# Performance work log

Hardware: AMD Instinct MI355X
Metric: run time of the kernel (lower is better)

## Reference

```python
import jax, jax.numpy as jnp
import numpy as np

B, N, C_CLASS, C_CHARGE, S_MAX = 128, 256, 5, 3, 300


def setup_inputs() -> dict:
    key = jax.random.key(0)
    ks = jax.random.split(key, 12)
    return {
        "particle_class": jax.random.randint(ks[0], (B, N), 0, C_CLASS),
        "particle_charge": jax.random.randint(ks[1], (B, N), 0, C_CHARGE),
        "n_particles": jax.random.randint(ks[2], (B,), 0, S_MAX),
        "pflow_class_logits": jax.random.normal(ks[3], (B, N, C_CLASS), jnp.float32),
        "pflow_charge_logits": jax.random.normal(ks[4], (B, N, C_CHARGE), jnp.float32),
        "particle_pos": jax.random.normal(ks[5], (B, N, 3), jnp.float32),
        "pflow_pos": jax.random.normal(ks[6], (B, N, 3), jnp.float32),
        "particle_mom": jax.random.normal(ks[7], (B, N, 3), jnp.float32),
        "pflow_mom": jax.random.normal(ks[8], (B, N, 3), jnp.float32),
        "particle_energy": jax.random.normal(ks[9], (B, N), jnp.float32),
        "pflow_energy": jax.random.normal(ks[10], (B, N), jnp.float32),
        "predicted_setsizes": jax.random.normal(ks[11], (B, N, S_MAX), jnp.float32),
    }


def _pairwise_nll(logits, labels):
    # logits: [B, Nq, C] (pflow/dst side), labels: [B, Np] int (particle/src side)
    # returns CE(dst_logits_j, src_label_i) for every pair -> [B, Np, Nq]
    logp = jax.nn.log_softmax(logits, axis=-1)            # [B, Nq, C]
    idx = labels[:, :, None, None]                        # [B, Np, 1, 1]
    return -jnp.take_along_axis(logp[:, None, :, :], idx, axis=3)[..., 0]


def reference(particle_class, particle_charge, n_particles,
              pflow_class_logits, pflow_charge_logits,
              particle_pos, pflow_pos, particle_mom, pflow_mom,
              particle_energy, pflow_energy, predicted_setsizes):
    # per-edge (full bipartite per event) pair losses -> [B, Np, Nq]
    class_l = _pairwise_nll(pflow_class_logits, particle_class)
    charge_l = _pairwise_nll(pflow_charge_logits, particle_charge)
    pos_l = jnp.linalg.norm(particle_pos[:, :, None, :] - pflow_pos[:, None, :, :], axis=-1)
    mom_l = jnp.linalg.norm(particle_mom[:, :, None, :] - pflow_mom[:, None, :, :], axis=-1)
    en_l = (particle_energy[:, :, None] - pflow_energy[:, None, :]) ** 2
    pair_loss = class_l + charge_l + pos_l + mom_l + en_l  # [B, Np, Nq]

    # segment-min over mailbox: per-pflow min over incoming particle edges,
    # per-particle min over incoming pflow edges
    min_per_pflow = pair_loss.min(axis=1)      # [B, Nq]
    min_per_particle = pair_loss.min(axis=2)   # [B, Np]

    particle_loss = min_per_particle.sum(axis=1).mean()
    pflow_loss = min_per_pflow.sum(axis=1).mean()

    # setsize: mean over pflow nodes per event, CE against true multiplicity
    setsize_logp = jax.nn.log_softmax(predicted_setsizes.mean(axis=1), axis=-1)  # [B, S]
    setsize_loss = -jnp.take_along_axis(setsize_logp, n_particles[:, None], axis=1)[:, 0].mean()

    loss = particle_loss + pflow_loss + setsize_loss
    return loss
```

## Files before the change

### kernel.cpp

```cpp
#include <hip/hip_runtime.h>
#include <math.h>

#define BQ 128
#define NQ 256
#define SMAX 300
#define CCLS 5
#define CCHG 3
#define TSTR 268
#define RSTR 12
#define INFV 3.0e38f

#define NBLK 256

#define W_COL 0
#define W_SC  65536
#define W_SS  65792

#define P_TAB   0
#define P_COLS  4020
#define P_ROWS  6068
#define P_RED   7604
#define P_PART  9652
#define SMEM_FLOATS 9656

__device__ __forceinline__ float fast_sqrtf(float x) {
    return __builtin_amdgcn_sqrtf(x);
}

__global__ __launch_bounds__(512, 2) void main_kernel(
    const int* __restrict__ p_class, const int* __restrict__ p_charge,
    const float* __restrict__ cls_logits, const float* __restrict__ chg_logits,
    const float* __restrict__ p_pos, const float* __restrict__ pf_pos,
    const float* __restrict__ p_mom, const float* __restrict__ pf_mom,
    const float* __restrict__ p_en, const float* __restrict__ pf_en,
    const float* __restrict__ setsizes, float* __restrict__ ws,
    float* __restrict__ out, int out_size)
{
    __shared__ float smem[SMEM_FLOATS];
    const int t   = threadIdx.x;
    const int blk = blockIdx.x;
    const int b   = blk >> 1;
    const int h   = blk & 1;
    const int base = b * NQ;

    float* s_tab  = smem + P_TAB;
    float* s_cols = smem + P_COLS;
    float* s_rows = smem + P_ROWS;
    float* s_red  = smem + P_RED;
    float* s_part = smem + P_PART;

    if (t < NQ) {
        const int gj = base + t;
        const float* cl = cls_logits + (size_t)gj * CCLS;
        float l0=cl[0], l1=cl[1], l2=cl[2], l3=cl[3], l4=cl[4];
        float mx = fmaxf(fmaxf(fmaxf(l0,l1),fmaxf(l2,l3)),l4);
        float lse = mx + __logf(__expf(l0-mx)+__expf(l1-mx)+__expf(l2-mx)+
                                __expf(l3-mx)+__expf(l4-mx));
        const float* gl = chg_logits + (size_t)gj * CCHG;
        float g0=gl[0], g1=gl[1], g2=gl[2];
        float gmx = fmaxf(fmaxf(g0,g1),g2);
        float glse = gmx + __logf(__expf(g0-gmx)+__expf(g1-gmx)+__expf(g2-gmx));
        float nc[CCLS] = {lse-l0, lse-l1, lse-l2, lse-l3, lse-l4};
        float ng[CCHG] = {glse-g0, glse-g1, glse-g2};
        #pragma unroll
        for (int c = 0; c < CCLS; ++c)
            #pragma unroll
            for (int g = 0; g < CCHG; ++g)
                s_tab[(c*CCHG+g)*TSTR + t] = nc[c] + ng[g];

        float* cr = &s_cols[t*8];
        cr[0]=pf_pos[gj*3+0]; cr[1]=pf_pos[gj*3+1]; cr[2]=pf_pos[gj*3+2];
        cr[3]=pf_mom[gj*3+0]; cr[4]=pf_mom[gj*3+1]; cr[5]=pf_mom[gj*3+2];
        cr[6]=pf_en[gj];      cr[7]=0.0f;
    } else if (t < NQ + 128) {
        const int rr = t - NQ;
        const int gr = base + h*128 + rr;
        float* rw = &s_rows[rr*RSTR];
        rw[0]=p_pos[gr*3+0]; rw[1]=p_pos[gr*3+1]; rw[2]=p_pos[gr*3+2];
        rw[3]=p_mom[gr*3+0]; rw[4]=p_mom[gr*3+1]; rw[5]=p_mom[gr*3+2];
        rw[6]=p_en[gr];
        rw[7]=__int_as_float(p_class[gr]*CCHG + p_charge[gr]);
    } else {
        if (blk == 0) {
            for (int i = t - (NQ + 128); i < out_size && i < 1024; i += 128)
                out[i] = 0.0f;
        }
    }
    __syncthreads();

    const int tx = t & 31;
    const int ty = t >> 5;
    const int c0 = ty * 16;

    float4 ra[4], rb[4];
    int ccr[4];
    #pragma unroll
    for (int r = 0; r < 4; ++r) {
        const int row = tx + 32*r;
        ra[r] = *(const float4*)&s_rows[row*RSTR];
        rb[r] = *(const float4*)&s_rows[row*RSTR + 4];
        ccr[r] = __float_as_int(rb[r].w) * TSTR;
    }
    float rmin[4] = {INFV, INFV, INFV, INFV};

    const bool ssa = (t < SMAX);
    const float* ssp = setsizes + ((size_t)base + (size_t)(h*128)) * SMAX + t;
    float ssacc = 0.0f;

    #pragma unroll 1
    for (int chunk = 0; chunk < 4; ++chunk) {
        float ssv[32];
        if (ssa) {
            #pragma unroll
            for (int u = 0; u < 32; ++u)
                ssv[u] = ssp[(size_t)(chunk*32 + u) * SMAX];
        }

        float cm[4] = {INFV, INFV, INFV, INFV};
        #pragma unroll
        for (int cc = 0; cc < 4; ++cc) {
            const int j = c0 + chunk*4 + cc;
            const float4 cd0 = *(const float4*)&s_cols[j*8];
            const float4 cd1 = *(const float4*)&s_cols[j*8+4];
            #pragma unroll
            for (int r = 0; r < 4; ++r) {
                float dx=ra[r].x-cd0.x, dy=ra[r].y-cd0.y, dz=ra[r].z-cd0.z;
                float ex=ra[r].w-cd0.w, ey=rb[r].x-cd1.x, ez=rb[r].y-cd1.y;
                float de=rb[r].z-cd1.z;
                float v = s_tab[ccr[r] + j]
                        + fast_sqrtf(dx*dx + dy*dy + dz*dz)
                        + fast_sqrtf(ex*ex + ey*ey + ez*ez)
                        + de*de;
                rmin[r] = fminf(rmin[r], v);
                cm[cc]  = fminf(cm[cc], v);
            }
        }

        #pragma unroll
        for (int cc = 0; cc < 4; ++cc) {
            float v = cm[cc];
            #pragma unroll
            for (int off = 16; off > 0; off >>= 1)
                v = fminf(v, __shfl_down(v, off, 32));
            if (tx == 0) ws[W_COL + blk*NQ + c0 + chunk*4 + cc] = v;
        }

        if (ssa) {
            #pragma unroll
            for (int u = 0; u < 32; ++u) ssacc += ssv[u];
        }
    }

    if (ssa) ws[W_SS + blk*304 + t] = ssacc;

    #pragma unroll
    for (int r = 0; r < 4; ++r)
        s_red[ty*128 + tx + 32*r] = rmin[r];
    __syncthreads();
    if (t < 128) {
        float m = s_red[t];
        #pragma unroll
        for (int k = 1; k < 16; ++k) m = fminf(m, s_red[k*128 + t]);
        #pragma unroll
        for (int off = 32; off > 0; off >>= 1) m += __shfl_down(m, off, 64);
        if ((t & 63) == 0) s_part[t >> 6] = m;
    }
    __syncthreads();
    if (t == 0)
        ws[W_SC + blk] = s_part[0] + s_part[1];
}

__global__ __launch_bounds__(512) void combine_kernel(
    const int* __restrict__ n_particles, const float* __restrict__ ws,
    float* __restrict__ out)
{
    __shared__ float s_p[8], s_q[8], s_m[304], s_one[1];
    const int b = blockIdx.x;
    const int t = threadIdx.x;
    const int wave = t >> 6, lane = t & 63;

    float v = 0.0f;
    if (t < NQ)
        v = fminf(ws[W_COL + (2*b)*NQ + t], ws[W_COL + (2*b+1)*NQ + t]);
    #pragma unroll
    for (int off = 32; off > 0; off >>= 1) v += __shfl_down(v, off, 64);
    if (lane == 0) s_p[wave] = v;

    float m = -INFV;
    if (t < SMAX) {
        m = (ws[W_SS + (2*b)*304 + t] + ws[W_SS + (2*b+1)*304 + t]) * (1.0f / NQ);
        s_m[t] = m;
    }
    float wm = m;
    #pragma unroll
    for (int off = 32; off > 0; off >>= 1) wm = fmaxf(wm, __shfl_down(wm, off, 64));
    if (lane == 0) s_q[wave] = wm;
    __syncthreads();
    if (t == 0) {
        float a = fmaxf(fmaxf(s_q[0], s_q[1]), fmaxf(s_q[2], s_q[3]));
        float c = fmaxf(fmaxf(s_q[4], s_q[5]), fmaxf(s_q[6], s_q[7]));
        s_one[0] = fmaxf(a, c);
    }
    __syncthreads();
    const float mx = s_one[0];
    float e = (t < SMAX) ? __expf(m - mx) : 0.0f;
    #pragma unroll
    for (int off = 32; off > 0; off >>= 1) e += __shfl_down(e, off, 64);
    if (lane == 0) s_q[wave] = e;
    __syncthreads();
    if (t == 0) {
        float S = s_q[0]+s_q[1]+s_q[2]+s_q[3]+s_q[4]+s_q[5]+s_q[6]+s_q[7];
        float colsum = s_p[0]+s_p[1]+s_p[2]+s_p[3]+s_p[4]+s_p[5]+s_p[6]+s_p[7];
        int nb = n_particles[b];
        float ssl = -(s_m[nb] - mx - __logf(S));
        float total = colsum + ws[W_SC + 2*b] + ws[W_SC + 2*b + 1] + ssl;
        atomicAdd(out, total * (1.0f / BQ));
    }
}

extern "C" void kernel_launch(void* const* d_in, const int* in_sizes, int n_in,
                              void* d_out, int out_size, void* d_ws, size_t ws_size,
                              hipStream_t stream) {
    (void)in_sizes; (void)n_in; (void)ws_size;
    const int*   p_class     = (const int*)d_in[0];
    const int*   p_charge    = (const int*)d_in[1];
    const int*   n_particles = (const int*)d_in[2];
    const float* cls_logits  = (const float*)d_in[3];
    const float* chg_logits  = (const float*)d_in[4];
    const float* p_pos       = (const float*)d_in[5];
    const float* pf_pos      = (const float*)d_in[6];
    const float* p_mom       = (const float*)d_in[7];
    const float* pf_mom      = (const float*)d_in[8];
    const float* p_en        = (const float*)d_in[9];
    const float* pf_en       = (const float*)d_in[10];
    const float* setsizes    = (const float*)d_in[11];
    float* out = (float*)d_out;
    float* ws  = (float*)d_ws;

    main_kernel<<<NBLK, 512, 0, stream>>>(
        p_class, p_charge, cls_logits, chg_logits,
        p_pos, pf_pos, p_mom, pf_mom, p_en, pf_en, setsizes, ws, out, out_size);

    combine_kernel<<<BQ, 512, 0, stream>>>(n_particles, ws, out);
}
```

Baseline: 110.5 us.

## Fuse combine kernel into main kernel via inter-block flag handoff

Removes the separate combine launch. The odd half-block of each event publishes its column minima, setsize sums and row-min sum to workspace and sets two magic-value flags. The even half-block spins on those flags, combines the values with its own shared-memory results, and publishes a per-event total. Block 0 then waits on all per-event flags and writes the final mean, replacing the atomicAdd and the separate zeroing of the output. The flags are never reset, so on repeated calls a waiting block may see the previous call's flags and read stale or partially written data. The design also relies on every block being co-resident to avoid deadlock.

```diff
diff --git a/kernel.cpp b/kernel.cpp
--- a/kernel.cpp
+++ b/kernel.cpp
@@ -13,22 +13,42 @@
 #define NBLK 256
 
 #define W_COL 0
-#define W_SC  65536
-#define W_SS  65792
+#define W_SC  32768
+#define W_SS  32896
+#define W_B   71808
+#define W_FA  71936
+#define W_FB  72064
+#define W_GA  72192
+#define W_GB  72320
+
+#define MAGIC_A 0x1F2E3D4Cu
+#define MAGIC_B 0xC4D3E2F1u
+#define MAGIC_C 0x0A1B2C3Du
+#define MAGIC_D 0xD3C2B1A0u
 
 #define P_TAB   0
 #define P_COLS  4020
 #define P_ROWS  6068
 #define P_RED   7604
 #define P_PART  9652
-#define SMEM_FLOATS 9656
+#define P_OWNC  9656
+#define P_OWNS  9912
+#define SMEM_FLOATS 10216
 
 __device__ __forceinline__ float fast_sqrtf(float x) {
     return __builtin_amdgcn_sqrtf(x);
 }
 
+__device__ __forceinline__ void pub(unsigned int* p, unsigned int v) {
+    __hip_atomic_store(p, v, __ATOMIC_RELEASE, __HIP_MEMORY_SCOPE_AGENT);
+}
+__device__ __forceinline__ unsigned int seen(const unsigned int* p) {
+    return __hip_atomic_load(p, __ATOMIC_ACQUIRE, __HIP_MEMORY_SCOPE_AGENT);
+}
+
 __global__ __launch_bounds__(512, 2) void main_kernel(
     const int* __restrict__ p_class, const int* __restrict__ p_charge,
+    const int* __restrict__ n_particles,
     const float* __restrict__ cls_logits, const float* __restrict__ chg_logits,
     const float* __restrict__ p_pos, const float* __restrict__ pf_pos,
     const float* __restrict__ p_mom, const float* __restrict__ pf_mom,
@@ -42,12 +62,15 @@
     const int b   = blk >> 1;
     const int h   = blk & 1;
     const int base = b * NQ;
+    unsigned int* wsu = (unsigned int*)ws;
 
     float* s_tab  = smem + P_TAB;
     float* s_cols = smem + P_COLS;
     float* s_rows = smem + P_ROWS;
     float* s_red  = smem + P_RED;
     float* s_part = smem + P_PART;
+    float* s_ownc = smem + P_OWNC;
+    float* s_owns = smem + P_OWNS;
 
     if (t < NQ) {
         const int gj = base + t;
@@ -80,11 +103,6 @@
         rw[3]=p_mom[gr*3+0]; rw[4]=p_mom[gr*3+1]; rw[5]=p_mom[gr*3+2];
         rw[6]=p_en[gr];
         rw[7]=__int_as_float(p_class[gr]*CCHG + p_charge[gr]);
-    } else {
-        if (blk == 0) {
-            for (int i = t - (NQ + 128); i < out_size && i < 1024; i += 128)
-                out[i] = 0.0f;
-        }
     }
     __syncthreads();
 
@@ -142,7 +160,10 @@
             #pragma unroll
             for (int off = 16; off > 0; off >>= 1)
                 v = fminf(v, __shfl_down(v, off, 32));
-            if (tx == 0) ws[W_COL + blk*NQ + c0 + chunk*4 + cc] = v;
+            if (tx == 0) {
+                s_ownc[c0 + chunk*4 + cc] = v;
+                if (h) ws[W_COL + b*NQ + c0 + chunk*4 + cc] = v;
+            }
         }
 
         if (ssa) {
@@ -151,7 +172,10 @@
         }
     }
 
-    if (ssa) ws[W_SS + blk*304 + t] = ssacc;
+    if (ssa) {
+        s_owns[t] = ssacc;
+        if (h) ws[W_SS + b*304 + t] = ssacc;
+    }
 
     #pragma unroll
     for (int r = 0; r < 4; ++r)
@@ -166,29 +190,42 @@
         if ((t & 63) == 0) s_part[t >> 6] = m;
     }
     __syncthreads();
-    if (t == 0)
-        ws[W_SC + blk] = s_part[0] + s_part[1];
-}
-
-__global__ __launch_bounds__(512) void combine_kernel(
-    const int* __restrict__ n_particles, const float* __restrict__ ws,
-    float* __restrict__ out)
-{
-    __shared__ float s_p[8], s_q[8], s_m[304], s_one[1];
-    const int b = blockIdx.x;
-    const int t = threadIdx.x;
+
+    float rs = s_part[0] + s_part[1];
+
+    if (h) {
+        if (t == 0) {
+            ws[W_SC + b] = rs;
+            __threadfence();
+            pub(&wsu[W_FA + b], MAGIC_A);
+            pub(&wsu[W_FB + b], MAGIC_B);
+        }
+        return;
+    }
+
+    if (t == 0) {
+        while (seen(&wsu[W_FA + b]) != MAGIC_A ||
+               seen(&wsu[W_FB + b]) != MAGIC_B) { }
+        __threadfence();
+    }
+    __syncthreads();
+
+    float* s_m   = smem;
+    float* s_p   = smem + 304;
+    float* s_q   = smem + 312;
+    float* s_one = smem + 320;
     const int wave = t >> 6, lane = t & 63;
 
     float v = 0.0f;
     if (t < NQ)
-        v = fminf(ws[W_COL + (2*b)*NQ + t], ws[W_COL + (2*b+1)*NQ + t]);
+        v = fminf(s_ownc[t], ws[W_COL + b*NQ + t]);
     #pragma unroll
     for (int off = 32; off > 0; off >>= 1) v += __shfl_down(v, off, 64);
     if (lane == 0) s_p[wave] = v;
 
     float m = -INFV;
     if (t < SMAX) {
-        m = (ws[W_SS + (2*b)*304 + t] + ws[W_SS + (2*b+1)*304 + t]) * (1.0f / NQ);
+        m = (s_owns[t] + ws[W_SS + b*304 + t]) * (1.0f / NQ);
         s_m[t] = m;
     }
     float wm = m;
@@ -213,9 +250,32 @@
         float colsum = s_p[0]+s_p[1]+s_p[2]+s_p[3]+s_p[4]+s_p[5]+s_p[6]+s_p[7];
         int nb = n_particles[b];
         float ssl = -(s_m[nb] - mx - __logf(S));
-        float total = colsum + ws[W_SC + 2*b] + ws[W_SC + 2*b + 1] + ssl;
-        atomicAdd(out, total * (1.0f / BQ));
-    }
+        float total = colsum + rs + ws[W_SC + b] + ssl;
+        ws[W_B + b] = total;
+        __threadfence();
+        pub(&wsu[W_GA + b], MAGIC_C);
+        pub(&wsu[W_GB + b], MAGIC_D);
+    }
+
+    if (blk != 0) return;
+
+    int ok;
+    do {
+        int mine = 1;
+        if (t < BQ)
+            mine = (seen(&wsu[W_GA + t]) == MAGIC_C) &&
+                   (seen(&wsu[W_GB + t]) == MAGIC_D);
+        ok = __syncthreads_and(mine);
+    } while (!ok);
+    __threadfence();
+
+    float tv = (t < BQ) ? ws[W_B + t] : 0.0f;
+    #pragma unroll
+    for (int off = 32; off > 0; off >>= 1) tv += __shfl_down(tv, off, 64);
+    if (lane == 0 && wave < 2) s_p[wave] = tv;
+    __syncthreads();
+    if (t == 0) out[0] = (s_p[0] + s_p[1]) * (1.0f / BQ);
+    for (int i = 1 + t; i < out_size && i < 1024; i += 512) out[i] = 0.0f;
 }
 
 extern "C" void kernel_launch(void* const* d_in, const int* in_sizes, int n_in,
@@ -238,8 +298,6 @@
     float* ws  = (float*)d_ws;
 
     main_kernel<<<NBLK, 512, 0, stream>>>(
-        p_class, p_charge, cls_logits, chg_logits,
+        p_class, p_charge, n_particles, cls_logits, chg_logits,
         p_pos, pf_pos, p_mom, pf_mom, p_en, pf_en, setsizes, ws, out, out_size);
-
-    combine_kernel<<<BQ, 512, 0, stream>>>(n_particles, ws, out);
-}
+}
```

After: 130.2 us. 1.18x slower.
